# Kernel tuning notes

Hardware: AMD Instinct MI355X
Metric: run time of the kernel (lower is better)

The kernel has to match this reference:

```python
import jax, jax.numpy as jnp
import numpy as np

N = 100000   # nodes
E = 1600000  # edges (before self loops)
IN, HID, HEADS, OUT = 128, 32, 2, 32


def setup_inputs() -> dict:
    key = jax.random.key(0)
    ks = jax.random.split(key, 10)
    def glorot(k, shape, fan_in):
        return jax.random.normal(k, shape, dtype=jnp.float32) / np.sqrt(fan_in)
    return {
        "x": jax.random.normal(ks[0], (N, IN), dtype=jnp.float32),
        "edge_index": jax.random.randint(ks[1], (2, E), 0, N, dtype=jnp.int32),
        "W1": glorot(ks[2], (IN, HEADS * HID), IN),
        "a_src1": glorot(ks[3], (HEADS, HID), HID),
        "a_dst1": glorot(ks[4], (HEADS, HID), HID),
        "b1": jnp.zeros((HEADS * HID,), dtype=jnp.float32),
        "W2": glorot(ks[5], (HEADS * HID, OUT), HEADS * HID),
        "a_src2": glorot(ks[6], (1, OUT), OUT),
        "a_dst2": glorot(ks[7], (1, OUT), OUT),
        "b2": jnp.zeros((OUT,), dtype=jnp.float32),
    }


def gat_conv(x, W, a_src, a_dst, b, src, dst, n):
    """PyG-style GATConv: shared linear, edge softmax over incoming edges, sum aggregate."""
    H, C = a_src.shape
    xl = (x @ W).reshape(n, H, C)                       # [N, H, C]
    asn = jnp.einsum('nhc,hc->nh', xl, a_src)            # per-node source score
    adn = jnp.einsum('nhc,hc->nh', xl, a_dst)            # per-node dest score
    e = jax.nn.leaky_relu(asn[src] + adn[dst], 0.2)      # [E', H]
    m = jax.ops.segment_max(e, dst, num_segments=n)      # stable softmax per dest
    m = jnp.where(jnp.isfinite(m), m, 0.0)
    ex = jnp.exp(e - m[dst])
    denom = jax.ops.segment_sum(ex, dst, num_segments=n)
    alpha = ex / (denom[dst] + 1e-16)                    # [E', H]
    out = jax.ops.segment_sum(xl[src] * alpha[:, :, None], dst, num_segments=n)
    return out.reshape(n, H * C) + b


def reference(x, edge_index, W1, a_src1, a_dst1, b1, W2, a_src2, a_dst2, b2):
    n = x.shape[0]
    loop = jnp.arange(n, dtype=edge_index.dtype)         # add self loops (PyG default)
    src = jnp.concatenate([edge_index[0], loop])
    dst = jnp.concatenate([edge_index[1], loop])
    h = jax.nn.relu(gat_conv(x, W1, a_src1, a_dst1, b1, src, dst, n))
    # F.dropout(p=0.5) is identity in eval mode
    return gat_conv(h, W2, a_src2, a_dst2, b2, src, dst, n)
```

## Files before the change

kernel.cpp:

```cpp
#include <hip/hip_runtime.h>
#include <hip/hip_fp16.h>


#define BS 256
#define PCHUNK 8192
#define CAPB 5632
#define GPAD 16

typedef _Float16 half8 __attribute__((ext_vector_type(8)));
typedef float f32x4 __attribute__((ext_vector_type(4)));

__global__ __launch_bounds__(BS) void k_init(int* __restrict__ gcursor, int nbuk) {
    for (int i = threadIdx.x; i < nbuk; i += BS) gcursor[i * GPAD] = i * CAPB;
}

__global__ __launch_bounds__(BS) void k_pg1(const int* __restrict__ ei, int E, int n,
                                            int* __restrict__ gcursor, int* __restrict__ ppair,
                                            const float* __restrict__ x, const float* __restrict__ W,
                                            const float* __restrict__ asrc, const float* __restrict__ adst,
                                            __half* __restrict__ xl, float* __restrict__ sc, int gC) {
    __shared__ _Float16 smem[8192];
    int tid = threadIdx.x;
    if ((int)blockIdx.x < gC) {
        int* cnt  = (int*)smem;
        int* gpos = cnt + 512;
        int* lcur = cnt + 1024;
        cnt[tid] = 0; cnt[tid + 256] = 0;
        lcur[tid] = 0; lcur[tid + 256] = 0;
        __syncthreads();
        const int* dstp = ei + E;
        int base = blockIdx.x * PCHUNK;
        bool full = (base + PCHUNK <= E);
        if (full) {
            const int4* dv = (const int4*)(dstp + base) + tid * 8;
#pragma unroll
            for (int k = 0; k < 8; k++) {
                int4 d4 = dv[k];
                atomicAdd(&cnt[d4.x >> 8], 1);
                atomicAdd(&cnt[d4.y >> 8], 1);
                atomicAdd(&cnt[d4.z >> 8], 1);
                atomicAdd(&cnt[d4.w >> 8], 1);
            }
        } else {
            for (int i = tid; base + i < E; i += BS)
                atomicAdd(&cnt[dstp[base + i] >> 8], 1);
        }
        __syncthreads();
        for (int b = tid; b < 512; b += BS) {
            int c = cnt[b];
            if (c > 0) gpos[b] = atomicAdd(&gcursor[b * GPAD], c);
        }
        __syncthreads();
        if (full) {
            const int4* sv = (const int4*)(ei + base) + tid * 8;
            const int4* dv = (const int4*)(dstp + base) + tid * 8;
#pragma unroll 2
            for (int k = 0; k < 8; k++) {
                int4 s4 = sv[k];
                int4 d4 = dv[k];
                int d, s, b, r;
                d = d4.x; s = s4.x; b = d >> 8; r = atomicAdd(&lcur[b], 1);
                ppair[gpos[b] + r] = ((d & 255) << 17) | s;
                d = d4.y; s = s4.y; b = d >> 8; r = atomicAdd(&lcur[b], 1);
                ppair[gpos[b] + r] = ((d & 255) << 17) | s;
                d = d4.z; s = s4.z; b = d >> 8; r = atomicAdd(&lcur[b], 1);
                ppair[gpos[b] + r] = ((d & 255) << 17) | s;
                d = d4.w; s = s4.w; b = d >> 8; r = atomicAdd(&lcur[b], 1);
                ppair[gpos[b] + r] = ((d & 255) << 17) | s;
            }
        } else {
            for (int i = tid; base + i < E; i += BS) {
                int s = ei[base + i], d = dstp[base + i];
                int b = d >> 8;
                int r = atomicAdd(&lcur[b], 1);
                ppair[gpos[b] + r] = ((d & 255) << 17) | s;
            }
        }
        return;
    }
    _Float16* wf = smem;
    for (int i = tid; i < 8192; i += BS) {
        int j = i & 7, ln = (i >> 3) & 63, f = i >> 9;
        int kt = f >> 2, nt = f & 3;
        int k = kt * 32 + (ln >> 4) * 8 + j;
        wf[i] = (_Float16)W[k * 64 + nt * 16 + (ln & 15)];
    }
    __syncthreads();
    int wave = tid >> 6, lane = tid & 63;
    int nb = ((blockIdx.x - gC) * 4 + wave) * 16;
    int m = lane & 15, q = lane >> 4;
    int node_m = nb + m; if (node_m >= n) node_m = n - 1;
    half8 bf[4][4];
#pragma unroll
    for (int f = 0; f < 16; f++)
        bf[f >> 2][f & 3] = *(half8*)&wf[(f * 64 + lane) * 8];
    f32x4 acc[4] = {f32x4{0,0,0,0}, f32x4{0,0,0,0}, f32x4{0,0,0,0}, f32x4{0,0,0,0}};
#pragma unroll
    for (int kt = 0; kt < 4; kt++) {
        const float* xp = x + (size_t)node_m * 128 + kt * 32 + q * 8;
        float4 xa = *(const float4*)xp;
        float4 xb = *(const float4*)(xp + 4);
        half8 a;
        a[0] = (_Float16)xa.x; a[1] = (_Float16)xa.y; a[2] = (_Float16)xa.z; a[3] = (_Float16)xa.w;
        a[4] = (_Float16)xb.x; a[5] = (_Float16)xb.y; a[6] = (_Float16)xb.z; a[7] = (_Float16)xb.w;
#pragma unroll
        for (int nt = 0; nt < 4; nt++)
            acc[nt] = __builtin_amdgcn_mfma_f32_16x16x32_f16(a, bf[kt][nt], acc[nt], 0, 0, 0);
    }
    int c = lane & 15;
    float a_s[4], a_d[4];
#pragma unroll
    for (int nt = 0; nt < 4; nt++) { a_s[nt] = asrc[nt * 16 + c]; a_d[nt] = adst[nt * 16 + c]; }
#pragma unroll
    for (int r = 0; r < 4; r++) {
        int node = nb + q * 4 + r;
        bool ok = node < n;
        float v0 = acc[0][r], v1 = acc[1][r], v2 = acc[2][r], v3 = acc[3][r];
        float as0 = v0 * a_s[0] + v1 * a_s[1];
        float as1 = v2 * a_s[2] + v3 * a_s[3];
        float ad0 = v0 * a_d[0] + v1 * a_d[1];
        float ad1 = v2 * a_d[2] + v3 * a_d[3];
#pragma unroll
        for (int off = 1; off < 16; off <<= 1) {
            as0 += __shfl_xor(as0, off); as1 += __shfl_xor(as1, off);
            ad0 += __shfl_xor(ad0, off); ad1 += __shfl_xor(ad1, off);
        }
        if (ok) {
            __half* row = xl + (size_t)node * 64;
            row[c]      = __float2half(v0);
            row[16 + c] = __float2half(v1);
            row[32 + c] = __float2half(v2);
            row[48 + c] = __float2half(v3);
            if (c == 0) ((float4*)sc)[node] = make_float4(as0, as1, ad0, ad1);
        }
    }
}

__global__ __launch_bounds__(BS) void k_bucket(const int* __restrict__ ppair,
                                               const int* __restrict__ gcursor, int n,
                                               int* __restrict__ col,
                                               int* __restrict__ row_ptr, int* __restrict__ row_end) {
    __shared__ int ldeg[256];
    __shared__ int lscan[256];
    __shared__ int lcur[256];
    __shared__ int lcol[CAPB];
    int b = blockIdx.x;
    int t = threadIdx.x;
    int lo = b << 8;
    int hi = lo + 256; if (hi > n) hi = n;
    int W = hi - lo;
    int base = b * CAPB;
    int cnt = gcursor[b * GPAD] - base;
    if (cnt > CAPB) cnt = CAPB;
    ldeg[t] = 0;
    __syncthreads();
    for (int i = t; i < cnt; i += BS)
        atomicAdd(&ldeg[ppair[base + i] >> 17], 1);
    __syncthreads();
    lscan[t] = ldeg[t];
    __syncthreads();
    for (int off = 1; off < 256; off <<= 1) {
        int a = (t >= off) ? lscan[t - off] : 0;
        __syncthreads();
        lscan[t] += a;
        __syncthreads();
    }
    {
        int e0 = lscan[t] - ldeg[t];
        lcur[t] = e0;
        if (t < W) { row_ptr[lo + t] = base + e0; row_end[lo + t] = base + e0 + ldeg[t]; }
    }
    __syncthreads();
    for (int i = t; i < cnt; i += BS) {
        int p = ppair[base + i];
        int r = atomicAdd(&lcur[p >> 17], 1);
        if (r < CAPB) lcol[r] = p & 131071;
    }
    __syncthreads();
    for (int i = t; i < cnt; i += BS) col[base + i] = lcol[i];
}

__global__ __launch_bounds__(BS) void k_ag1g2(const int* __restrict__ row_ptr, const int* __restrict__ row_end,
                                              const int* __restrict__ col, const __half* __restrict__ xl,
                                              const float* __restrict__ sc, const float* __restrict__ asrc,
                                              const float* __restrict__ b1,
                                              const float* __restrict__ W2,
                                              const float* __restrict__ as2, const float* __restrict__ ad2,
                                              __half* __restrict__ xl2, float* __restrict__ sc2, int n) {
    __shared__ _Float16 hsh[32 * 72];
    __shared__ _Float16 wf2[2048];
    int tid = threadIdx.x;
    for (int i = tid; i < 2048; i += BS) {
        int j = i & 7, ln = (i >> 3) & 63, f = i >> 9;
        int kt = f >> 1, nt = f & 1;
        int k = kt * 32 + (ln >> 4) * 8 + j;
        wf2[i] = (_Float16)W2[k * 32 + nt * 16 + (ln & 15)];
    }
    int node_local = tid >> 3;
    int node = blockIdx.x * 32 + node_local;
    int tc = tid & 7;
    int lane = tid & 63;
    int tb = lane & 56;
    bool alive = node < n;
    int nodeC = alive ? node : n - 1;
    float4 acA = ((const float4*)asrc)[tc * 2];
    float4 acB = ((const float4*)asrc)[tc * 2 + 1];
    int s0 = row_ptr[nodeC], e1 = row_end[nodeC];
    float4 sn = ((const float4*)sc)[nodeC];
    bool hh0 = tc < 4;
    float adn = hh0 ? sn.z : sn.w;
    float es0 = sn.x + sn.z; es0 = fmaxf(es0, 0.2f * es0);
    float es1 = sn.y + sn.w; es1 = fmaxf(es1, 0.2f * es1);
    float xs = __expf(hh0 ? es0 : es1);
    uint4 rawS = *(const uint4*)(xl + (size_t)nodeC * 64 + tc * 8);
    __half2 sh0 = *(__half2*)&rawS.x, sh1 = *(__half2*)&rawS.y;
    __half2 sh2 = *(__half2*)&rawS.z, sh3 = *(__half2*)&rawS.w;
    float acc0 = xs * __low2float(sh0), acc1 = xs * __high2float(sh0);
    float acc2 = xs * __low2float(sh1), acc3 = xs * __high2float(sh1);
    float acc4 = xs * __low2float(sh2), acc5 = xs * __high2float(sh2);
    float acc6 = xs * __low2float(sh3), acc7 = xs * __high2float(sh3);
    float den = xs;
    int deg = e1 - s0;
    int mx = deg;
    mx = max(mx, __shfl_xor(mx, 8));
    mx = max(mx, __shfl_xor(mx, 16));
    mx = max(mx, __shfl_xor(mx, 32));
    int nch = (mx + 7) >> 3;
    for (int ci = 0; ci < nch; ci++) {
        int pos = s0 + ci * 8;
        int m = e1 - pos; m = m < 0 ? 0 : (m > 8 ? 8 : m);
        int srcv = (tc < m) ? col[pos + tc] : 0;
#pragma unroll
        for (int kb = 0; kb < 8; kb += 4) {
            int rem = m - kb;
            if (rem > 0) {
                int nv = rem < 4 ? rem : 4;
                uint4 rr[4];
#pragma unroll
                for (int k = 0; k < 4; k++) {
                    if (k < nv) {
                        int sE = __shfl(srcv, tb + kb + k);
                        rr[k] = *(const uint4*)(xl + (size_t)sE * 64 + tc * 8);
                    }
                }
#pragma unroll
                for (int k = 0; k < 4; k++) {
                    if (k < nv) {
                        __half2 q0 = *(__half2*)&rr[k].x, q1 = *(__half2*)&rr[k].y;
                        __half2 q2 = *(__half2*)&rr[k].z, q3 = *(__half2*)&rr[k].w;
                        float f0 = __low2float(q0), f1 = __high2float(q0);
                        float f2 = __low2float(q1), f3 = __high2float(q1);
                        float f4 = __low2float(q2), f5 = __high2float(q2);
                        float f6 = __low2float(q3), f7 = __high2float(q3);
                        float dA = f0 * acA.x + f1 * acA.y + f2 * acA.z + f3 * acA.w;
                        float dB = f4 * acB.x + f5 * acB.y + f6 * acB.z + f7 * acB.w;
                        float dot = dA + dB;
                        dot += __shfl_xor(dot, 1);
                        dot += __shfl_xor(dot, 2);
                        float e = dot + adn; e = fmaxf(e, 0.2f * e);
                        float w = __expf(e);
                        acc0 = fmaf(w, f0, acc0); acc1 = fmaf(w, f1, acc1);
                        acc2 = fmaf(w, f2, acc2); acc3 = fmaf(w, f3, acc3);
                        acc4 = fmaf(w, f4, acc4); acc5 = fmaf(w, f5, acc5);
                        acc6 = fmaf(w, f6, acc6); acc7 = fmaf(w, f7, acc7);
                        den += w;
                    }
                }
            }
        }
    }
    float dinv = 1.f / (den + 1e-16f);
    {
        float4 bvA = ((const float4*)b1)[tc * 2];
        float4 bvB = ((const float4*)b1)[tc * 2 + 1];
        __half2 p0 = __floats2half2_rn(fmaxf(fmaf(acc0, dinv, bvA.x), 0.f),
                                       fmaxf(fmaf(acc1, dinv, bvA.y), 0.f));
        __half2 p1 = __floats2half2_rn(fmaxf(fmaf(acc2, dinv, bvA.z), 0.f),
                                       fmaxf(fmaf(acc3, dinv, bvA.w), 0.f));
        __half2 p2 = __floats2half2_rn(fmaxf(fmaf(acc4, dinv, bvB.x), 0.f),
                                       fmaxf(fmaf(acc5, dinv, bvB.y), 0.f));
        __half2 p3 = __floats2half2_rn(fmaxf(fmaf(acc6, dinv, bvB.z), 0.f),
                                       fmaxf(fmaf(acc7, dinv, bvB.w), 0.f));
        uint4 o;
        o.x = *(unsigned int*)&p0; o.y = *(unsigned int*)&p1;
        o.z = *(unsigned int*)&p2; o.w = *(unsigned int*)&p3;
        *(uint4*)&hsh[node_local * 72 + tc * 8] = o;
    }
    __syncthreads();
    int wave = tid >> 6;
    if (wave < 2) {
        int m2 = lane & 15, q2 = lane >> 4;
        int nl = wave * 16 + m2;
        half8 bf[2][2];
#pragma unroll
        for (int f = 0; f < 4; f++)
            bf[f >> 1][f & 1] = *(half8*)&wf2[(f * 64 + lane) * 8];
        f32x4 acc2g[2] = {f32x4{0,0,0,0}, f32x4{0,0,0,0}};
#pragma unroll
        for (int kt = 0; kt < 2; kt++) {
            half8 a = *(half8*)&hsh[nl * 72 + kt * 32 + q2 * 8];
#pragma unroll
            for (int nt = 0; nt < 2; nt++)
                acc2g[nt] = __builtin_amdgcn_mfma_f32_16x16x32_f16(a, bf[kt][nt], acc2g[nt], 0, 0, 0);
        }
        int c = lane & 15;
        float a_s[2], a_d[2];
#pragma unroll
        for (int nt = 0; nt < 2; nt++) { a_s[nt] = as2[nt * 16 + c]; a_d[nt] = ad2[nt * 16 + c]; }
#pragma unroll
        for (int r = 0; r < 4; r++) {
            int nl_r = wave * 16 + q2 * 4 + r;
            int node_r = blockIdx.x * 32 + nl_r;
            bool ok = node_r < n;
            float v0 = acc2g[0][r], v1 = acc2g[1][r];
            float as = v0 * a_s[0] + v1 * a_s[1];
            float ad = v0 * a_d[0] + v1 * a_d[1];
#pragma unroll
            for (int off = 1; off < 16; off <<= 1) {
                as += __shfl_xor(as, off); ad += __shfl_xor(ad, off);
            }
            if (ok) {
                __half* row = xl2 + (size_t)node_r * 32;
                row[c]      = __float2half(v0);
                row[16 + c] = __float2half(v1);
                if (c == 0) ((float2*)sc2)[node_r] = make_float2(as, ad);
            }
        }
    }
}

__global__ __launch_bounds__(BS) void k_agg2(const int* __restrict__ row_ptr, const int* __restrict__ row_end,
                                             const int* __restrict__ col, const __half* __restrict__ xl,
                                             const float* __restrict__ sc, const float* __restrict__ asrc,
                                             const float* __restrict__ b2,
                                             float* __restrict__ out, int n) {
    int tid = blockIdx.x * BS + threadIdx.x;
    int node = tid >> 2;
    int tc = threadIdx.x & 3;
    int lane = threadIdx.x & 63;
    int tb = lane & 60;
    bool alive = node < n;
    if (!alive) node = n - 1;
    float4 acA = ((const float4*)asrc)[tc * 2];
    float4 acB = ((const float4*)asrc)[tc * 2 + 1];
    int s0 = row_ptr[node], e1 = row_end[node];
    float2 sn = ((const float2*)sc)[node];
    float adn = sn.y;
    float es = sn.x + adn; es = fmaxf(es, 0.2f * es);
    float xs = __expf(es);
    uint4 rawS = *(const uint4*)(xl + (size_t)node * 32 + tc * 8);
    __half2 sh0 = *(__half2*)&rawS.x, sh1 = *(__half2*)&rawS.y;
    __half2 sh2 = *(__half2*)&rawS.z, sh3 = *(__half2*)&rawS.w;
    float acc0 = xs * __low2float(sh0), acc1 = xs * __high2float(sh0);
    float acc2 = xs * __low2float(sh1), acc3 = xs * __high2float(sh1);
    float acc4 = xs * __low2float(sh2), acc5 = xs * __high2float(sh2);
    float acc6 = xs * __low2float(sh3), acc7 = xs * __high2float(sh3);
    float den = xs;
    int deg = e1 - s0;
    int mx = deg;
    mx = max(mx, __shfl_xor(mx, 4));
    mx = max(mx, __shfl_xor(mx, 8));
    mx = max(mx, __shfl_xor(mx, 16));
    mx = max(mx, __shfl_xor(mx, 32));
    int nch = (mx + 3) >> 2;
    for (int ci = 0; ci < nch; ci++) {
        int pos = s0 + ci * 4;
        int m = e1 - pos; m = m < 0 ? 0 : (m > 4 ? 4 : m);
        int srcv = (tc < m) ? col[pos + tc] : 0;
        if (m > 0) {
            uint4 rr[4];
#pragma unroll
            for (int k = 0; k < 4; k++) {
                if (k < m) {
                    int sE = __shfl(srcv, tb + k);
                    rr[k] = *(const uint4*)(xl + (size_t)sE * 32 + tc * 8);
                }
            }
#pragma unroll
            for (int k = 0; k < 4; k++) {
                if (k < m) {
                    __half2 q0 = *(__half2*)&rr[k].x, q1 = *(__half2*)&rr[k].y;
                    __half2 q2 = *(__half2*)&rr[k].z, q3 = *(__half2*)&rr[k].w;
                    float f0 = __low2float(q0), f1 = __high2float(q0);
                    float f2 = __low2float(q1), f3 = __high2float(q1);
                    float f4 = __low2float(q2), f5 = __high2float(q2);
                    float f6 = __low2float(q3), f7 = __high2float(q3);
                    float dA = f0 * acA.x + f1 * acA.y + f2 * acA.z + f3 * acA.w;
                    float dB = f4 * acB.x + f5 * acB.y + f6 * acB.z + f7 * acB.w;
                    float dot = dA + dB;
                    dot += __shfl_xor(dot, 1);
                    dot += __shfl_xor(dot, 2);
                    float e = dot + adn; e = fmaxf(e, 0.2f * e);
                    float w = __expf(e);
                    acc0 = fmaf(w, f0, acc0); acc1 = fmaf(w, f1, acc1);
                    acc2 = fmaf(w, f2, acc2); acc3 = fmaf(w, f3, acc3);
                    acc4 = fmaf(w, f4, acc4); acc5 = fmaf(w, f5, acc5);
                    acc6 = fmaf(w, f6, acc6); acc7 = fmaf(w, f7, acc7);
                    den += w;
                }
            }
        }
    }
    float dinv = 1.f / (den + 1e-16f);
    if (alive) {
        float4 bvA = ((const float4*)b2)[tc * 2];
        float4 bvB = ((const float4*)b2)[tc * 2 + 1];
        float4 oA, oB;
        oA.x = fmaf(acc0, dinv, bvA.x);
        oA.y = fmaf(acc1, dinv, bvA.y);
        oA.z = fmaf(acc2, dinv, bvA.z);
        oA.w = fmaf(acc3, dinv, bvA.w);
        oB.x = fmaf(acc4, dinv, bvB.x);
        oB.y = fmaf(acc5, dinv, bvB.y);
        oB.z = fmaf(acc6, dinv, bvB.z);
        oB.w = fmaf(acc7, dinv, bvB.w);
        float4* orow = (float4*)(out + (size_t)node * 32);
        orow[tc * 2]     = oA;
        orow[tc * 2 + 1] = oB;
    }
}

extern "C" void kernel_launch(void* const* d_in, const int* in_sizes, int n_in,
                              void* d_out, int out_size, void* d_ws, size_t ws_size,
                              hipStream_t stream) {
    const float* x    = (const float*)d_in[0];
    const int*   ei   = (const int*)d_in[1];
    const float* W1   = (const float*)d_in[2];
    const float* as1  = (const float*)d_in[3];
    const float* ad1  = (const float*)d_in[4];
    const float* b1   = (const float*)d_in[5];
    const float* W2   = (const float*)d_in[6];
    const float* as2  = (const float*)d_in[7];
    const float* ad2  = (const float*)d_in[8];
    const float* b2   = (const float*)d_in[9];
    int n = in_sizes[0] / 128;
    int E = in_sizes[1] / 2;
    int NBUK = (n + 255) >> 8;

    char* w = (char*)d_ws;
    auto alloc = [&](size_t bytes) -> char* {
        char* p = w; w += (bytes + 255) / 256 * 256; return p;
    };
    int*    gcursor = (int*)alloc((size_t)NBUK * GPAD * 4);
    int*    ppair   = (int*)alloc((size_t)NBUK * CAPB * 4);
    int*    col     = (int*)alloc((size_t)NBUK * CAPB * 4);
    int*    row_ptr = (int*)alloc((size_t)n * 4);
    int*    row_end = (int*)alloc((size_t)n * 4);
    __half* xl1     = (__half*)alloc((size_t)n * 64 * 2);
    float*  sc1     = (float*)alloc((size_t)n * 4 * 4);
    __half* xl2     = (__half*)alloc((size_t)n * 32 * 2);
    float*  sc2     = (float*)alloc((size_t)n * 2 * 4);

    int gC  = (E + PCHUNK - 1) / PCHUNK;
    int gG  = (n + 63) / 64;
    int gA1 = (n * 8 + BS - 1) / BS;
    int gA2 = (n * 4 + BS - 1) / BS;

    k_init   <<<1, BS, 0, stream>>>(gcursor, NBUK);
    k_pg1    <<<gC + gG, BS, 0, stream>>>(ei, E, n, gcursor, ppair,
                                          x, W1, as1, ad1, xl1, sc1, gC);
    k_bucket <<<NBUK, BS, 0, stream>>>(ppair, gcursor, n, col, row_ptr, row_end);
    k_ag1g2  <<<gA1, BS, 0, stream>>>(row_ptr, row_end, col, xl1, sc1, as1, b1,
                                      W2, as2, ad2, xl2, sc2, n);
    k_agg2   <<<gA2, BS, 0, stream>>>(row_ptr, row_end, col, xl2, sc2, as2, b2,
                                      (float*)d_out, n);
}
```

Measured before the change: 218.6 us.

## Sort nodes by in-degree into a permutation to balance aggregation waves

Builds a degree histogram in the bucket kernel and adds a scatter kernel that produces a node permutation ordered by descending in-degree. Both aggregation kernels now walk nodes through this permutation, so lanes in a wave handle nodes of similar degree and the wave's loop trip count (max degree across lanes) matches its workload better. The price is an extra kernel launch, a histogram pass, an indirection on node lookups, and scattered output writes and feature reads in place of contiguous ones.

```diff
diff --git a/kernel.cpp b/kernel.cpp
--- a/kernel.cpp
+++ b/kernel.cpp
@@ -6,12 +6,16 @@
 #define PCHUNK 8192
 #define CAPB 5632
 #define GPAD 16
+#define DBIN(d) (63 - ((d) < 63 ? (d) : 63))
 
 typedef _Float16 half8 __attribute__((ext_vector_type(8)));
 typedef float f32x4 __attribute__((ext_vector_type(4)));
 
-__global__ __launch_bounds__(BS) void k_init(int* __restrict__ gcursor, int nbuk) {
-    for (int i = threadIdx.x; i < nbuk; i += BS) gcursor[i * GPAD] = i * CAPB;
+__global__ __launch_bounds__(BS) void k_init(int* __restrict__ gcursor, int nbuk,
+                                             int* __restrict__ dhist, int* __restrict__ dcur) {
+    int t = threadIdx.x;
+    for (int i = t; i < nbuk; i += BS) gcursor[i * GPAD] = i * CAPB;
+    if (t < 64) { dhist[t * GPAD] = 0; dcur[t * GPAD] = 0; }
 }
 
 __global__ __launch_bounds__(BS) void k_pg1(const int* __restrict__ ei, int E, int n,
@@ -139,10 +143,12 @@
 __global__ __launch_bounds__(BS) void k_bucket(const int* __restrict__ ppair,
                                                const int* __restrict__ gcursor, int n,
                                                int* __restrict__ col,
-                                               int* __restrict__ row_ptr, int* __restrict__ row_end) {
+                                               int* __restrict__ row_ptr, int* __restrict__ row_end,
+                                               int* __restrict__ dhist) {
     __shared__ int ldeg[256];
     __shared__ int lscan[256];
     __shared__ int lcur[256];
+    __shared__ int dbh[64];
     __shared__ int lcol[CAPB];
     int b = blockIdx.x;
     int t = threadIdx.x;
@@ -153,10 +159,12 @@
     int cnt = gcursor[b * GPAD] - base;
     if (cnt > CAPB) cnt = CAPB;
     ldeg[t] = 0;
+    if (t < 64) dbh[t] = 0;
     __syncthreads();
     for (int i = t; i < cnt; i += BS)
         atomicAdd(&ldeg[ppair[base + i] >> 17], 1);
     __syncthreads();
+    if (t < W) atomicAdd(&dbh[DBIN(ldeg[t])], 1);
     lscan[t] = ldeg[t];
     __syncthreads();
     for (int off = 1; off < 256; off <<= 1) {
@@ -169,6 +177,7 @@
         int e0 = lscan[t] - ldeg[t];
         lcur[t] = e0;
         if (t < W) { row_ptr[lo + t] = base + e0; row_end[lo + t] = base + e0 + ldeg[t]; }
+        if (t < 64 && dbh[t] > 0) atomicAdd(&dhist[t * GPAD], dbh[t]);
     }
     __syncthreads();
     for (int i = t; i < cnt; i += BS) {
@@ -178,6 +187,42 @@
     }
     __syncthreads();
     for (int i = t; i < cnt; i += BS) col[base + i] = lcol[i];
+}
+
+__global__ __launch_bounds__(BS) void k_dscat(const int* __restrict__ row_ptr,
+                                              const int* __restrict__ row_end,
+                                              const int* __restrict__ dhist, int* __restrict__ dcur,
+                                              int* __restrict__ perm, int n) {
+    __shared__ int ldh[64];
+    __shared__ int pref[64];
+    __shared__ int lh[64];
+    __shared__ int gb[64];
+    __shared__ int lc[64];
+    int t = threadIdx.x;
+    if (t < 64) { ldh[t] = dhist[t * GPAD]; lh[t] = 0; }
+    __syncthreads();
+    if (t < 64) {
+        int s = 0;
+        for (int b = 0; b < t; b++) s += ldh[b];
+        pref[t] = s;
+    }
+    int i = blockIdx.x * BS + t;
+    int bin = -1;
+    if (i < n) {
+        bin = DBIN(row_end[i] - row_ptr[i]);
+        atomicAdd(&lh[bin], 1);
+    }
+    __syncthreads();
+    if (t < 64) {
+        int c = lh[t];
+        gb[t] = c > 0 ? atomicAdd(&dcur[t * GPAD], c) : 0;
+        lc[t] = 0;
+    }
+    __syncthreads();
+    if (i < n) {
+        int r = atomicAdd(&lc[bin], 1);
+        perm[pref[bin] + gb[bin] + r] = i;
+    }
 }
 
 __global__ __launch_bounds__(BS) void k_ag1g2(const int* __restrict__ row_ptr, const int* __restrict__ row_end,
@@ -186,10 +231,16 @@
                                               const float* __restrict__ b1,
                                               const float* __restrict__ W2,
                                               const float* __restrict__ as2, const float* __restrict__ ad2,
+                                              const int* __restrict__ perm,
                                               __half* __restrict__ xl2, float* __restrict__ sc2, int n) {
     __shared__ _Float16 hsh[32 * 72];
     __shared__ _Float16 wf2[2048];
+    __shared__ int pslot[32];
     int tid = threadIdx.x;
+    if (tid < 32) {
+        int s = blockIdx.x * 32 + tid;
+        pslot[tid] = (s < n) ? perm[s] : -1;
+    }
     for (int i = tid; i < 2048; i += BS) {
         int j = i & 7, ln = (i >> 3) & 63, f = i >> 9;
         int kt = f >> 1, nt = f & 1;
@@ -197,12 +248,12 @@
         wf2[i] = (_Float16)W2[k * 32 + nt * 16 + (ln & 15)];
     }
     int node_local = tid >> 3;
-    int node = blockIdx.x * 32 + node_local;
+    int slot = blockIdx.x * 32 + node_local;
     int tc = tid & 7;
     int lane = tid & 63;
     int tb = lane & 56;
-    bool alive = node < n;
-    int nodeC = alive ? node : n - 1;
+    bool alive = slot < n;
+    int nodeC = alive ? perm[slot] : (n - 1);
     float4 acA = ((const float4*)asrc)[tc * 2];
     float4 acB = ((const float4*)asrc)[tc * 2 + 1];
     int s0 = row_ptr[nodeC], e1 = row_end[nodeC];
@@ -310,8 +361,8 @@
 #pragma unroll
         for (int r = 0; r < 4; r++) {
             int nl_r = wave * 16 + q2 * 4 + r;
-            int node_r = blockIdx.x * 32 + nl_r;
-            bool ok = node_r < n;
+            int node_r = pslot[nl_r];
+            bool ok = node_r >= 0;
             float v0 = acc2g[0][r], v1 = acc2g[1][r];
             float as = v0 * a_s[0] + v1 * a_s[1];
             float ad = v0 * a_d[0] + v1 * a_d[1];
@@ -333,14 +384,15 @@
                                              const int* __restrict__ col, const __half* __restrict__ xl,
                                              const float* __restrict__ sc, const float* __restrict__ asrc,
                                              const float* __restrict__ b2,
+                                             const int* __restrict__ perm,
                                              float* __restrict__ out, int n) {
     int tid = blockIdx.x * BS + threadIdx.x;
-    int node = tid >> 2;
+    int slot = tid >> 2;
     int tc = threadIdx.x & 3;
     int lane = threadIdx.x & 63;
     int tb = lane & 60;
-    bool alive = node < n;
-    if (!alive) node = n - 1;
+    bool alive = slot < n;
+    int node = alive ? perm[slot] : (n - 1);
     float4 acA = ((const float4*)asrc)[tc * 2];
     float4 acB = ((const float4*)asrc)[tc * 2 + 1];
     int s0 = row_ptr[node], e1 = row_end[node];
@@ -450,18 +502,23 @@
     float*  sc1     = (float*)alloc((size_t)n * 4 * 4);
     __half* xl2     = (__half*)alloc((size_t)n * 32 * 2);
     float*  sc2     = (float*)alloc((size_t)n * 2 * 4);
+    int*    dhist   = (int*)alloc(64 * GPAD * 4);
+    int*    dcur    = (int*)alloc(64 * GPAD * 4);
+    int*    perm    = (int*)alloc((size_t)n * 4);
 
     int gC  = (E + PCHUNK - 1) / PCHUNK;
     int gG  = (n + 63) / 64;
+    int gDS = (n + BS - 1) / BS;
     int gA1 = (n * 8 + BS - 1) / BS;
     int gA2 = (n * 4 + BS - 1) / BS;
 
-    k_init   <<<1, BS, 0, stream>>>(gcursor, NBUK);
+    k_init   <<<1, BS, 0, stream>>>(gcursor, NBUK, dhist, dcur);
     k_pg1    <<<gC + gG, BS, 0, stream>>>(ei, E, n, gcursor, ppair,
                                           x, W1, as1, ad1, xl1, sc1, gC);
-    k_bucket <<<NBUK, BS, 0, stream>>>(ppair, gcursor, n, col, row_ptr, row_end);
+    k_bucket <<<NBUK, BS, 0, stream>>>(ppair, gcursor, n, col, row_ptr, row_end, dhist);
+    k_dscat  <<<gDS, BS, 0, stream>>>(row_ptr, row_end, dhist, dcur, perm, n);
     k_ag1g2  <<<gA1, BS, 0, stream>>>(row_ptr, row_end, col, xl1, sc1, as1, b1,
-                                      W2, as2, ad2, xl2, sc2, n);
+                                      W2, as2, ad2, perm, xl2, sc2, n);
     k_agg2   <<<gA2, BS, 0, stream>>>(row_ptr, row_end, col, xl2, sc2, as2, b2,
-                                      (float*)d_out, n);
-}
+                                      perm, (float*)d_out, n);
+}
```

Result: slower. 236.5 us (+8.2%).
